# Kernel tuning notes

Hardware: AMD Instinct MI355X
Metric: run time of the kernel (lower is better)

## Reference

```python
import jax, jax.numpy as jnp
import numpy as np
from jax import lax

B, N, HID = 2, 2048, 2048
H, KVH, D = 16, 4, 128           # heads, kv heads, head_dim
GROUPS = H // KVH
FLA_WEIGHT = 0.01
NEG = -1e30


def setup_inputs() -> dict:
    key = jax.random.key(0)
    ks = jax.random.split(key, 5)
    s = 0.02
    return {
        "hidden_states": jax.random.normal(ks[0], (B, N, HID), jnp.float32),
        "Wq": jax.random.normal(ks[1], (HID, H * D), jnp.float32) * s,
        "Wk": jax.random.normal(ks[2], (HID, KVH * D), jnp.float32) * s,
        "Wv": jax.random.normal(ks[3], (HID, KVH * D), jnp.float32) * s,
        "Wo": jax.random.normal(ks[4], (H * D, HID), jnp.float32) * s,
    }


def _split_heads(x, h):
    b, n, _ = x.shape
    return x.reshape(b, n, h, -1).transpose(0, 2, 1, 3)  # b h n d


def _gla_attention(q, k, v, scale):
    # Gated linear attention: S_t = sigmoid(k_t) (.) S_{t-1} + k_t (x) v_t,
    # o_t = scale * q_t . S_t ; sequential recurrence over the seq dim.
    qs = jnp.moveaxis(q, 2, 0)  # n b h d
    ks = jnp.moveaxis(k, 2, 0)
    vs = jnp.moveaxis(v, 2, 0)

    def step(S, inp):
        qt, kt, vt = inp                                   # each (b,h,d)
        g = jax.nn.sigmoid(kt)                             # per-key-dim gate
        S = S * g[..., None] + kt[..., None] * vt[..., None, :]  # (b,h,d,dv)
        ot = scale * jnp.einsum('bhd,bhde->bhe', qt, S)
        return S, ot

    S0 = jnp.zeros(q.shape[:2] + (q.shape[-1], v.shape[-1]), q.dtype)
    _, o = lax.scan(step, S0, (qs, ks, vs))                # n b h dv
    return jnp.moveaxis(o, 0, 2)                           # b h n dv


def reference(hidden_states, Wq, Wk, Wv, Wo):
    scale = 1.0 / np.sqrt(D)
    q = _split_heads(hidden_states @ Wq, H)                # b h n d
    k = _split_heads(hidden_states @ Wk, KVH)
    v = _split_heads(hidden_states @ Wv, KVH)
    k = jnp.repeat(k, GROUPS, axis=1)                      # repeat_kv -> b H n d
    v = jnp.repeat(v, GROUPS, axis=1)

    # FLA branch
    fla = _gla_attention(q, k, v, scale)                   # b h n d
    fla = fla.transpose(0, 2, 1, 3).reshape(B, N, H * D)   # b n (h d)

    # Base causal softmax attention
    scores = jnp.einsum('bhnd,bhmd->bhnm', q, k) * scale
    causal = jnp.tril(jnp.ones((N, N), bool))
    scores = jnp.where(causal, scores, NEG)
    attn = jax.nn.softmax(scores, axis=-1)
    base = jnp.einsum('bhnm,bhmd->bhnd', attn, v)
    base = base.transpose(0, 2, 1, 3).reshape(B, N, H * D) @ Wo

    return base + FLA_WEIGHT * fla
```

## Files before the change

kernel.cpp:

```cpp
#include <hip/hip_runtime.h>
#include <hip/hip_bf16.h>
#include <cstdint>
#include <cstddef>


typedef __attribute__((ext_vector_type(4))) float f32x4;
typedef __attribute__((ext_vector_type(2))) float f32x2;
typedef __attribute__((ext_vector_type(8))) short s16x8;
typedef unsigned short u16;
typedef unsigned int u32;

__device__ __forceinline__ float bfu2f(u16 u) {
  union { unsigned int i; float f; } x; x.i = ((unsigned int)u) << 16; return x.f;
}
__device__ __forceinline__ u16 f2bfu(float f) {
  union { float f; unsigned int i; } x; x.f = f;
  unsigned int r = x.i + 0x7fffu + ((x.i >> 16) & 1u);
  return (u16)(r >> 16);
}
__device__ __forceinline__ void bf8_to_f(s16x8 v, float* o) {
  union { s16x8 v; u16 u[8]; } x; x.v = v;
#pragma unroll
  for (int j = 0; j < 8; j++) o[j] = bfu2f(x.u[j]);
}
__device__ __forceinline__ s16x8 pack_bf8(f32x4 lo, f32x4 hi) {
  union { s16x8 v; u16 u[8]; } x;
#pragma unroll
  for (int j = 0; j < 4; j++) { x.u[j] = f2bfu(lo[j]); x.u[4 + j] = f2bfu(hi[j]); }
  return x.v;
}
__device__ __forceinline__ void gload_lds16(const u16* g, u16* l) {
  __builtin_amdgcn_global_load_lds(
      (__attribute__((address_space(1))) void*)(g),
      (__attribute__((address_space(3))) void*)(l), 16, 0, 0);
}

__global__ __launch_bounds__(256) void f32_to_bf16(
    const float* __restrict__ src, u16* __restrict__ dst, int n8) {
  const int i = blockIdx.x * 256 + threadIdx.x;
  if (i < n8) {
    f32x4 a = *(const f32x4*)(src + (size_t)i * 8);
    f32x4 b = *(const f32x4*)(src + (size_t)i * 8 + 4);
    *(s16x8*)(dst + (size_t)i * 8) = pack_bf8(a, b);
  }
}

__global__ __launch_bounds__(256) void transpose_f32_bf16(
    const float* __restrict__ src, u16* __restrict__ dst, int R, int C) {
  __shared__ u16 tile[32][33];
  const int bx = blockIdx.x * 32, by = blockIdx.y * 32;
  const int tx = threadIdx.x & 31, ty = threadIdx.x >> 5;
#pragma unroll
  for (int i = 0; i < 32; i += 8)
    tile[ty + i][tx] = f2bfu(src[(size_t)(by + ty + i) * C + bx + tx]);
  __syncthreads();
#pragma unroll
  for (int i = 0; i < 32; i += 8)
    dst[(size_t)(bx + ty + i) * R + by + tx] = tile[tx][ty + i];
}

__global__ __launch_bounds__(256) void transpose_bf16(
    const u16* __restrict__ src, u16* __restrict__ dst, int R, int C) {
  __shared__ u16 tile[32][33];
  const int bx = blockIdx.x * 32, by = blockIdx.y * 32;
  const int tx = threadIdx.x & 31, ty = threadIdx.x >> 5;
#pragma unroll
  for (int i = 0; i < 32; i += 8)
    tile[ty + i][tx] = src[(size_t)(by + ty + i) * C + bx + tx];
  __syncthreads();
#pragma unroll
  for (int i = 0; i < 32; i += 8)
    dst[(size_t)(bx + ty + i) * R + by + tx] = tile[tx][ty + i];
}

__global__ __launch_bounds__(256) void gemm_qkv(
    const u16* __restrict__ A, const u16* __restrict__ WqT, const u16* __restrict__ WkT,
    const u16* __restrict__ WvT, u16* __restrict__ Qo, u16* __restrict__ Ko,
    u16* __restrict__ Vo) {
  __shared__ u16 Al[128 * 32];
  __shared__ u16 Bl[128 * 32];
  const int bx = blockIdx.x;
  const u16* Bt; u16* Cb; int n0, Nst;
  if (bx < 16)      { Bt = WqT; Cb = Qo; n0 = bx * 128;        Nst = 2048; }
  else if (bx < 20) { Bt = WkT; Cb = Ko; n0 = (bx - 16) * 128; Nst = 512; }
  else              { Bt = WvT; Cb = Vo; n0 = (bx - 20) * 128; Nst = 512; }
  const int K = 2048;
  const int m0 = blockIdx.y * 128;
  const int t = threadIdx.x, w = t >> 6, l = t & 63, lm = l & 15, lq = l >> 4;
  const int wr = w >> 1, wc = w & 1;
  const f32x4 z4 = {0.f, 0.f, 0.f, 0.f};
  f32x4 acc[4][4];
#pragma unroll
  for (int i = 0; i < 4; i++)
#pragma unroll
    for (int j = 0; j < 4; j++) acc[i][j] = z4;
  const int srow = l >> 2, scol = (l & 3) * 8;
  const u16* Ag = A + (size_t)(m0 + w * 32 + srow) * K + scol;
  const u16* Bg = Bt + (size_t)(n0 + w * 32 + srow) * K + scol;
  u16* Alw = &Al[(w * 32) * 32];
  u16* Blw = &Bl[(w * 32) * 32];
  for (int kk = 0; kk < K; kk += 32) {
    gload_lds16(Ag + kk, Alw);
    gload_lds16(Ag + (size_t)16 * K + kk, Alw + 16 * 32);
    gload_lds16(Bg + kk, Blw);
    gload_lds16(Bg + (size_t)16 * K + kk, Blw + 16 * 32);
    __syncthreads();
    s16x8 af[4], bfr[4];
#pragma unroll
    for (int sm = 0; sm < 4; sm++) af[sm] = *(const s16x8*)&Al[(wr * 64 + sm * 16 + lm) * 32 + lq * 8];
#pragma unroll
    for (int sn = 0; sn < 4; sn++) bfr[sn] = *(const s16x8*)&Bl[(wc * 64 + sn * 16 + lm) * 32 + lq * 8];
#pragma unroll
    for (int sm = 0; sm < 4; sm++)
#pragma unroll
      for (int sn = 0; sn < 4; sn++)
        acc[sm][sn] = __builtin_amdgcn_mfma_f32_16x16x32_bf16(af[sm], bfr[sn], acc[sm][sn], 0, 0, 0);
    __syncthreads();
  }
#pragma unroll
  for (int sm = 0; sm < 4; sm++)
#pragma unroll
    for (int sn = 0; sn < 4; sn++)
#pragma unroll
      for (int r = 0; r < 4; r++) {
        const int row = m0 + wr * 64 + sm * 16 + lq * 4 + r;
        const int col = n0 + wc * 64 + sn * 16 + lm;
        Cb[(size_t)row * Nst + col] = f2bfu(acc[sm][sn][r]);
      }
}

__global__ __launch_bounds__(512) void gemm_out2(
    const u16* __restrict__ A, const u16* __restrict__ Bt, float* __restrict__ Cf,
    const u16* __restrict__ addsrc) {
  __shared__ u16 Abuf[3 * 16384];
  __shared__ u16 Bbuf[3 * 8192];
  int f = blockIdx.y * 16 + blockIdx.x;
  f = (f & 7) * 32 + (f >> 3);
  const int by = f >> 4, bx = f & 15;
  const int m0 = by * 256, n0 = bx * 128;
  const int K = 2048, Nst = 2048;
  const int t = threadIdx.x, w = t >> 6, l = t & 63, lm = l & 15, lq = l >> 4;
  const int wr = w >> 1, wc = w & 1;
  const int tr = t >> 3, tc8 = (t & 7) * 8;
  const f32x4 z4 = {0.f, 0.f, 0.f, 0.f};
  f32x4 acc[4][4];
#pragma unroll
  for (int i = 0; i < 4; i++)
#pragma unroll
    for (int j = 0; j < 4; j++) acc[i][j] = z4;
  const u16* Ag = A + (size_t)m0 * K;
  const u16* Bg = Bt + (size_t)n0 * K;
  auto stage = [&](int kt, int bufi) {
#pragma unroll
    for (int i = 0; i < 4; i++) {
      const int row = i * 64 + tr;
      const int col = tc8 ^ ((row & 7) << 3);
      gload_lds16(Ag + (size_t)row * K + kt * 64 + col,
                  Abuf + bufi * 16384 + i * 4096 + w * 512);
    }
#pragma unroll
    for (int i = 0; i < 2; i++) {
      const int row = i * 64 + tr;
      const int col = tc8 ^ ((row & 7) << 3);
      gload_lds16(Bg + (size_t)row * K + kt * 64 + col,
                  Bbuf + bufi * 8192 + i * 4096 + w * 512);
    }
  };
  const int nt = K >> 6;
  stage(0, 0);
  stage(1, 1);
  int cur = 0;
#pragma unroll 1
  for (int kt = 0; kt < nt; kt++) {
    if (kt + 2 < nt) {
      int nb = cur + 2; if (nb >= 3) nb -= 3;
      stage(kt + 2, nb);
      asm volatile("s_waitcnt vmcnt(12)" ::: "memory");
    } else if (kt + 1 < nt) {
      asm volatile("s_waitcnt vmcnt(6)" ::: "memory");
    } else {
      asm volatile("s_waitcnt vmcnt(0)" ::: "memory");
    }
    __builtin_amdgcn_s_barrier();
    const u16* Ab = Abuf + cur * 16384;
    const u16* Bb = Bbuf + cur * 8192;
    s16x8 af[4][2], bff[4][2];
#pragma unroll
    for (int sm = 0; sm < 4; sm++) {
      const int row = wr * 64 + sm * 16 + lm;
#pragma unroll
      for (int kk = 0; kk < 2; kk++)
        af[sm][kk] = *(const s16x8*)&Ab[row * 64 +
            ((((kk << 6) | (lq << 4)) ^ ((row & 7) << 4)) >> 1)];
    }
#pragma unroll
    for (int sn = 0; sn < 4; sn++) {
      const int row = wc * 64 + sn * 16 + lm;
#pragma unroll
      for (int kk = 0; kk < 2; kk++)
        bff[sn][kk] = *(const s16x8*)&Bb[row * 64 +
            ((((kk << 6) | (lq << 4)) ^ ((row & 7) << 4)) >> 1)];
    }
#pragma unroll
    for (int kk = 0; kk < 2; kk++)
#pragma unroll
      for (int sm = 0; sm < 4; sm++)
#pragma unroll
        for (int sn = 0; sn < 4; sn++)
          acc[sm][sn] = __builtin_amdgcn_mfma_f32_16x16x32_bf16(
              af[sm][kk], bff[sn][kk], acc[sm][sn], 0, 0, 0);
    asm volatile("s_waitcnt lgkmcnt(0)" ::: "memory");
    __builtin_amdgcn_s_barrier();
    cur = (cur == 2) ? 0 : cur + 1;
  }
#pragma unroll
  for (int sm = 0; sm < 4; sm++)
#pragma unroll
    for (int sn = 0; sn < 4; sn++)
#pragma unroll
      for (int r = 0; r < 4; r++) {
        const int row = m0 + wr * 64 + sm * 16 + lq * 4 + r;
        const int col = n0 + wc * 64 + sn * 16 + lm;
        float v = acc[sm][sn][r] + 0.01f * bfu2f(addsrc[(size_t)row * Nst + col]);
        Cf[(size_t)row * Nst + col] = v;
      }
}

__global__ __launch_bounds__(512) void flash_attn_wave(
    const u16* __restrict__ Q, const u16* __restrict__ Kx,
    const u16* __restrict__ Vt, u16* __restrict__ AO) {
  __shared__ u16 Klds[2][64 * 128];
  __shared__ u16 Vlds[2][128 * 64];
  __shared__ u16 Pl[8][16][68];
  const int bid = blockIdx.x;
  const int set = bid & 7;
  const int b = set >> 2, kvh = set & 3;
  const int rest = bid >> 3;
  const int j0 = rest >> 1, hp = rest & 1;
  const int t = threadIdx.x, w = t >> 6, l = t & 63, lm = l & 15, lq = l >> 4;
  const int h = kvh * 4 + hp * 2 + (w & 1);
  const int cs = (w >> 1) & 1, mh = w >> 2;
  const float scale = 0.0883883476483184f;
  const u16* Kbase = Kx + (size_t)(b * 2048) * 512 + kvh * 128;
  const u16* Vbase = Vt + (size_t)(b * 512 + kvh * 128) * 2048;
  const f32x4 z4 = {0.f, 0.f, 0.f, 0.f};

  auto stage = [&](int kt, int bufi) {
    const int key0 = kt * 64;
#pragma unroll
    for (int r = 0; r < 2; r++) {
      const int row = r * 32 + w * 4 + (l >> 4);
      const int scb = ((l & 15) * 16) ^ ((row & 7) << 4);
      gload_lds16(Kbase + (size_t)(key0 + row) * 512 + (scb >> 1),
                  &Klds[bufi][r * 4096 + w * 512]);
    }
#pragma unroll
    for (int r = 0; r < 2; r++) {
      const int row = r * 64 + w * 8 + (l >> 3);
      const int scb = ((l & 7) * 16) ^ ((row & 7) << 4);
      gload_lds16(Vbase + (size_t)row * 2048 + key0 + (scb >> 1),
                  &Vlds[bufi][r * 4096 + w * 512]);
    }
  };

#pragma unroll 1
  for (int ph = 0; ph < 2; ph++) {
    const int j = ph ? (31 - j0) : j0;
    const int c = 2 * j + cs;
    const int base = c * 32;
    int cur = 0;
    stage(0, 0);
    s16x8 qf[4];
#pragma unroll
    for (int kk = 0; kk < 4; kk++)
      qf[kk] = *(const s16x8*)(Q + ((size_t)(b * 2048 + base + mh * 16 + lm)) * 2048 +
                               h * 128 + kk * 32 + lq * 8);
    f32x4 oacc[8];
#pragma unroll
    for (int e = 0; e < 8; e++) oacc[e] = z4;
    float lsum[4] = {0.f, 0.f, 0.f, 0.f};
#pragma unroll 1
    for (int kt = 0; kt <= j; kt++) {
      const int key0 = kt * 64;
      if (kt < j) {
        stage(kt + 1, cur ^ 1);
        asm volatile("s_waitcnt vmcnt(4)" ::: "memory");
      } else {
        asm volatile("s_waitcnt vmcnt(0)" ::: "memory");
      }
      __builtin_amdgcn_s_barrier();
      const char* KB = (const char*)&Klds[cur][0];
      const char* VB = (const char*)&Vlds[cur][0];
      s16x8 kf[4][4];
#pragma unroll
      for (int nst = 0; nst < 4; nst++)
#pragma unroll
        for (int kk = 0; kk < 4; kk++) {
          const int row = nst * 16 + lm;
          const int cb = (kk * 64 + lq * 16) ^ ((row & 7) << 4);
          kf[nst][kk] = *(const s16x8*)(KB + row * 256 + cb);
        }
      f32x4 sacc[4];
#pragma unroll
      for (int i = 0; i < 4; i++) sacc[i] = z4;
#pragma unroll
      for (int nst = 0; nst < 4; nst++)
#pragma unroll
        for (int kk = 0; kk < 4; kk++)
          sacc[nst] = __builtin_amdgcn_mfma_f32_16x16x32_bf16(
              qf[kk], kf[nst][kk], sacc[nst], 0, 0, 0);
      const bool diag = (kt == j);
#pragma unroll
      for (int r = 0; r < 4; r++) {
        const int qrow = base + mh * 16 + lq * 4 + r;
#pragma unroll
        for (int nst = 0; nst < 4; nst++) {
          float pv = __expf(sacc[nst][r] * scale);
          if (diag && (key0 + nst * 16 + lm > qrow)) pv = 0.f;
          lsum[r] += pv;
          Pl[w][lq * 4 + r][nst * 16 + lm] = f2bfu(pv);
        }
      }
      s16x8 vf[8][2];
#pragma unroll
      for (int et = 0; et < 8; et++)
#pragma unroll
        for (int kc = 0; kc < 2; kc++) {
          const int row = et * 16 + lm;
          const int cb = (kc * 64 + lq * 16) ^ ((row & 7) << 4);
          vf[et][kc] = *(const s16x8*)(VB + row * 128 + cb);
        }
      s16x8 pf[2];
#pragma unroll
      for (int kc = 0; kc < 2; kc++)
        pf[kc] = *(const s16x8*)&Pl[w][lm][kc * 32 + lq * 8];
#pragma unroll
      for (int et = 0; et < 8; et++)
#pragma unroll
        for (int kc = 0; kc < 2; kc++)
          oacc[et] = __builtin_amdgcn_mfma_f32_16x16x32_bf16(
              pf[kc], vf[et][kc], oacc[et], 0, 0, 0);
      asm volatile("s_waitcnt lgkmcnt(0)" ::: "memory");
      __builtin_amdgcn_s_barrier();
      cur ^= 1;
    }
#pragma unroll
    for (int r = 0; r < 4; r++) {
#pragma unroll
      for (int off = 1; off < 16; off <<= 1)
        lsum[r] += __shfl_xor(lsum[r], off, 64);
    }
#pragma unroll
    for (int r = 0; r < 4; r++) {
      const float inv = 1.f / lsum[r];
      const int row = base + mh * 16 + lq * 4 + r;
      u16* op = AO + ((size_t)(b * 2048 + row)) * 2048 + h * 128;
#pragma unroll
      for (int et = 0; et < 8; et++) op[et * 16 + lm] = f2bfu(oacc[et][r] * inv);
    }
  }
}

__global__ __launch_bounds__(256) void fla_contrib32(
    const u16* __restrict__ Kx, const u16* __restrict__ Vt,
    u16* __restrict__ Gg, u16* __restrict__ Ktg, u16* __restrict__ MT,
    float* __restrict__ Lam) {
  __shared__ float gl[32][132];
  __shared__ float kl[32][132];
  __shared__ float ktl[32][132];
  __shared__ u16 khT[128][40];
  const int c = blockIdx.x, kvh = blockIdx.y, b = blockIdx.z;
  const int bk = b * 4 + kvh;
  const int t = threadIdx.x;
  const size_t cb = (size_t)bk * 64 + c;
  {
    const int r = t >> 3, c0 = (t & 7) * 16;
    const u16* kp = Kx + ((size_t)(b * 2048 + c * 32 + r)) * 512 + kvh * 128 + c0;
#pragma unroll
    for (int i = 0; i < 2; i++) {
      float kv[8];
      bf8_to_f(*(const s16x8*)(kp + i * 8), kv);
#pragma unroll
      for (int j = 0; j < 8; j++) {
        kl[r][c0 + i * 8 + j] = kv[j];
        gl[r][c0 + i * 8 + j] = 1.f / (1.f + __expf(-kv[j]));
      }
    }
  }
  __syncthreads();
  if (t < 128) {
    float G = 1.f;
#pragma unroll
    for (int s = 0; s < 32; s++) {
      G *= gl[s][t];
      gl[s][t] = G;
      ktl[s][t] = kl[s][t] / G;
    }
    Lam[cb * 128 + t] = G;
    const float lam = G;
#pragma unroll
    for (int s = 0; s < 32; s++) khT[t][s] = f2bfu(ktl[s][t] * lam);
  }
  __syncthreads();
  {
    const int r = t >> 3, c0 = (t & 7) * 16;
    u16* gp = Gg + cb * 4096 + r * 128 + c0;
    u16* kp = Ktg + cb * 4096 + r * 128 + c0;
#pragma unroll
    for (int i = 0; i < 2; i++) {
      f32x4 a = *(f32x4*)&gl[r][c0 + i * 8];
      f32x4 b2 = *(f32x4*)&gl[r][c0 + i * 8 + 4];
      *(s16x8*)(gp + i * 8) = pack_bf8(a, b2);
      a = *(f32x4*)&ktl[r][c0 + i * 8];
      b2 = *(f32x4*)&ktl[r][c0 + i * 8 + 4];
      *(s16x8*)(kp + i * 8) = pack_bf8(a, b2);
    }
  }
  const int w = t >> 6, l = t & 63, lm = l & 15, lq = l >> 4;
  const f32x4 z4 = {0.f, 0.f, 0.f, 0.f};
  f32x4 macc[2][8];
#pragma unroll
  for (int ei = 0; ei < 2; ei++)
#pragma unroll
    for (int dt = 0; dt < 8; dt++) macc[ei][dt] = z4;
  s16x8 vtf[2];
#pragma unroll
  for (int ei = 0; ei < 2; ei++) {
    const int et = w * 2 + ei;
    vtf[ei] = *(const s16x8*)(Vt + ((size_t)(b * 512 + kvh * 128 + et * 16 + lm)) * 2048 +
                              c * 32 + lq * 8);
  }
#pragma unroll
  for (int dt = 0; dt < 8; dt++) {
    s16x8 kf = *(const s16x8*)&khT[dt * 16 + lm][lq * 8];
#pragma unroll
    for (int ei = 0; ei < 2; ei++)
      macc[ei][dt] = __builtin_amdgcn_mfma_f32_16x16x32_bf16(vtf[ei], kf, macc[ei][dt], 0, 0, 0);
  }
  u16* mp = MT + cb * 16384;
#pragma unroll
  for (int ei = 0; ei < 2; ei++)
#pragma unroll
    for (int dt = 0; dt < 8; dt++)
#pragma unroll
      for (int r = 0; r < 4; r++)
        mp[(size_t)((w * 2 + ei) * 16 + lq * 4 + r) * 128 + dt * 16 + lm] =
            f2bfu(macc[ei][dt][r]);
}

__global__ __launch_bounds__(256) void fla_prefix32(
    const u16* __restrict__ MT, const float* __restrict__ Lam, u16* __restrict__ SwsT) {
  const int eg = blockIdx.x, bk = blockIdx.y;
  const int t = threadIdx.x;
  const int e = eg * 4 + (t >> 6), d0 = (t & 63) * 2;
  const size_t cb0 = (size_t)bk * 64;
  const u16* mp = MT + cb0 * 16384 + e * 128 + d0;
  const float* lp = Lam + cb0 * 128 + d0;
  u16* sp = SwsT + cb0 * 16384 + e * 128 + d0;
  float s0 = 0.f, s1 = 0.f;
  u32 mnext = *(const u32*)mp;
  f32x2 lnext = *(const f32x2*)lp;
#pragma unroll 1
  for (int c = 0; c < 64; c++) {
    const u32 mcur = mnext;
    const f32x2 lcur = lnext;
    if (c < 63) {
      mnext = *(const u32*)(mp + (size_t)(c + 1) * 16384);
      lnext = *(const f32x2*)(lp + (size_t)(c + 1) * 128);
    }
    *(u32*)(sp + (size_t)c * 16384) = (u32)f2bfu(s0) | ((u32)f2bfu(s1) << 16);
    s0 = s0 * lcur[0] + bfu2f((u16)(mcur & 0xffffu));
    s1 = s1 * lcur[1] + bfu2f((u16)(mcur >> 16));
  }
}

__global__ __launch_bounds__(256) void fla_output_mfma(
    const u16* __restrict__ Q, const u16* __restrict__ Gg, const u16* __restrict__ Ktg,
    const u16* __restrict__ SwsT, const u16* __restrict__ Vt, u16* __restrict__ Fla) {
  __shared__ u16 Pl[4][2][16][40];
  const int c = blockIdx.x, h = blockIdx.y, b = blockIdx.z;
  const int kvh = h >> 2, bk = b * 4 + kvh;
  const int t = threadIdx.x, w = t >> 6, l = t & 63, lm = l & 15, lq = l >> 4;
  const float scale = 0.0883883476483184f;
  const size_t cb = (size_t)bk * 64 + c;
  const f32x4 z4 = {0.f, 0.f, 0.f, 0.f};
  s16x8 qgf[2][4];
#pragma unroll
  for (int m = 0; m < 2; m++)
#pragma unroll
    for (int kk = 0; kk < 4; kk++) {
      float qv[8], gv[8];
      bf8_to_f(*(const s16x8*)(Q + ((size_t)(b * 2048 + c * 32 + m * 16 + lm)) * 2048 +
                               h * 128 + kk * 32 + lq * 8), qv);
      bf8_to_f(*(const s16x8*)(Gg + cb * 4096 + (m * 16 + lm) * 128 + kk * 32 + lq * 8), gv);
      f32x4 a, b2;
#pragma unroll
      for (int j = 0; j < 4; j++) { a[j] = qv[j] * gv[j]; b2[j] = qv[4 + j] * gv[4 + j]; }
      qgf[m][kk] = pack_bf8(a, b2);
    }
  f32x4 sacc[2][2];
#pragma unroll
  for (int m = 0; m < 2; m++)
#pragma unroll
    for (int st = 0; st < 2; st++) sacc[m][st] = z4;
#pragma unroll
  for (int st = 0; st < 2; st++)
#pragma unroll
    for (int kk = 0; kk < 4; kk++) {
      s16x8 ktf = *(const s16x8*)(Ktg + cb * 4096 + (st * 16 + lm) * 128 + kk * 32 + lq * 8);
#pragma unroll
      for (int m = 0; m < 2; m++)
        sacc[m][st] = __builtin_amdgcn_mfma_f32_16x16x32_bf16(qgf[m][kk], ktf, sacc[m][st], 0, 0, 0);
    }
#pragma unroll
  for (int m = 0; m < 2; m++)
#pragma unroll
    for (int st = 0; st < 2; st++)
#pragma unroll
      for (int r = 0; r < 4; r++) {
        const int trow = m * 16 + lq * 4 + r;
        const int scol = st * 16 + lm;
        Pl[w][m][lq * 4 + r][st * 16 + lm] = f2bfu(scol <= trow ? sacc[m][st][r] : 0.f);
      }
  s16x8 pf[2];
#pragma unroll
  for (int m = 0; m < 2; m++) pf[m] = *(const s16x8*)&Pl[w][m][lm][lq * 8];
  f32x4 oacc[2][2];
#pragma unroll
  for (int m = 0; m < 2; m++)
#pragma unroll
    for (int ei = 0; ei < 2; ei++) oacc[m][ei] = z4;
#pragma unroll
  for (int ei = 0; ei < 2; ei++) {
    const int et = w * 2 + ei;
    s16x8 vtf = *(const s16x8*)(Vt + ((size_t)(b * 512 + kvh * 128 + et * 16 + lm)) * 2048 +
                                c * 32 + lq * 8);
#pragma unroll
    for (int m = 0; m < 2; m++)
      oacc[m][ei] = __builtin_amdgcn_mfma_f32_16x16x32_bf16(pf[m], vtf, oacc[m][ei], 0, 0, 0);
#pragma unroll
    for (int kk = 0; kk < 4; kk++) {
      s16x8 s0f = *(const s16x8*)(SwsT + cb * 16384 + (et * 16 + lm) * 128 + kk * 32 + lq * 8);
#pragma unroll
      for (int m = 0; m < 2; m++)
        oacc[m][ei] = __builtin_amdgcn_mfma_f32_16x16x32_bf16(qgf[m][kk], s0f, oacc[m][ei], 0, 0, 0);
    }
  }
#pragma unroll
  for (int m = 0; m < 2; m++)
#pragma unroll
    for (int ei = 0; ei < 2; ei++)
#pragma unroll
      for (int r = 0; r < 4; r++)
        Fla[((size_t)(b * 2048 + c * 32 + m * 16 + lq * 4 + r)) * 2048 + h * 128 +
            (w * 2 + ei) * 16 + lm] = f2bfu(scale * oacc[m][ei][r]);
}

extern "C" void kernel_launch(void* const* d_in, const int* in_sizes, int n_in,
                              void* d_out, int out_size, void* d_ws, size_t ws_size,
                              hipStream_t stream) {
  const float* X  = (const float*)d_in[0];
  const float* Wq = (const float*)d_in[1];
  const float* Wk = (const float*)d_in[2];
  const float* Wv = (const float*)d_in[3];
  const float* Wo = (const float*)d_in[4];
  float* out = (float*)d_out;

  char* ws = (char*)d_ws;
  size_t off = 0;
  auto alloc = [&](size_t bytes) { void* p = ws + off; off += (bytes + 255) & ~(size_t)255; return p; };
  u16* WoT = (u16*)alloc(2048ull * 2048 * 2);
  u16* Qb  = (u16*)alloc(4096ull * 2048 * 2);
  u16* Kb  = (u16*)alloc(4096ull * 512 * 2);
  u16* Vb  = (u16*)alloc(4096ull * 512 * 2);
  u16* Vtb = (u16*)alloc(2ull * 512 * 2048 * 2);
  u16* Fla = (u16*)alloc(4096ull * 2048 * 2);
  u16* SH16 = (u16*)alloc(4096ull * 2048 * 2);
  u16* Xb = SH16;
  u16* MT = SH16;
  u16* AO = SH16;
  char* BIG = (char*)alloc(26ull * 1024 * 1024);
  u16* WqT = (u16*)BIG;
  u16* WkT = (u16*)(BIG + 8ull * 1024 * 1024);
  u16* WvT = (u16*)(BIG + 10ull * 1024 * 1024);
  u16* Gg   = (u16*)BIG;
  u16* Ktg  = (u16*)(BIG + 4194304ull);
  u16* SwsT = (u16*)(BIG + 8388608ull);
  float* Lam = (float*)(BIG + 8388608ull + 16777216ull);
  (void)ws_size; (void)in_sizes; (void)n_in; (void)out_size;

  dim3 blk(256);
  f32_to_bf16<<<dim3(4096), blk, 0, stream>>>(X, Xb, 4096 * 2048 / 8);
  transpose_f32_bf16<<<dim3(64, 64), blk, 0, stream>>>(Wq, WqT, 2048, 2048);
  transpose_f32_bf16<<<dim3(16, 64), blk, 0, stream>>>(Wk, WkT, 2048, 512);
  transpose_f32_bf16<<<dim3(16, 64), blk, 0, stream>>>(Wv, WvT, 2048, 512);
  transpose_f32_bf16<<<dim3(64, 64), blk, 0, stream>>>(Wo, WoT, 2048, 2048);

  gemm_qkv<<<dim3(24, 32), blk, 0, stream>>>(Xb, WqT, WkT, WvT, Qb, Kb, Vb);

  transpose_bf16<<<dim3(16, 64), blk, 0, stream>>>(Vb, Vtb, 2048, 512);
  transpose_bf16<<<dim3(16, 64), blk, 0, stream>>>(Vb + 2048ull * 512, Vtb + 512ull * 2048, 2048, 512);

  fla_contrib32<<<dim3(64, 4, 2), blk, 0, stream>>>(Kb, Vtb, Gg, Ktg, MT, Lam);
  fla_prefix32<<<dim3(32, 8), blk, 0, stream>>>(MT, Lam, SwsT);
  fla_output_mfma<<<dim3(64, 16, 2), blk, 0, stream>>>(Qb, Gg, Ktg, SwsT, Vtb, Fla);

  flash_attn_wave<<<dim3(256), dim3(512), 0, stream>>>(Qb, Kb, Vtb, AO);

  gemm_out2<<<dim3(16, 16), dim3(512), 0, stream>>>(AO, WoT, out, Fla);
}
```

Before: 363.6 us.

## Split flash attention into 256-thread blocks per head and unroll prefix scan

Each flash attention block now handles one query head with 4 waves instead of two heads with 8 waves, and the grid doubles to 512 blocks. The aim is more blocks per CU, better latency hiding and better balance, at the cost of loading each K/V tile twice as often. The softmax exponent switches from __expf to exp2f with the scale folded into a log2(e) multiplier. The prefix-scan kernel is unrolled by two with two chunks prefetched ahead, to overlap its loads with the serial recurrence.

```diff
diff --git a/kernel.cpp b/kernel.cpp
--- a/kernel.cpp
+++ b/kernel.cpp
@@ -226,21 +226,22 @@
       }
 }
 
-__global__ __launch_bounds__(512) void flash_attn_wave(
+__global__ __launch_bounds__(256) void flash_attn_wave(
     const u16* __restrict__ Q, const u16* __restrict__ Kx,
     const u16* __restrict__ Vt, u16* __restrict__ AO) {
   __shared__ u16 Klds[2][64 * 128];
   __shared__ u16 Vlds[2][128 * 64];
-  __shared__ u16 Pl[8][16][68];
+  __shared__ u16 Pl[4][16][68];
   const int bid = blockIdx.x;
   const int set = bid & 7;
   const int b = set >> 2, kvh = set & 3;
   const int rest = bid >> 3;
-  const int j0 = rest >> 1, hp = rest & 1;
+  const int j0 = rest & 15;
+  const int hpq = rest >> 4;
   const int t = threadIdx.x, w = t >> 6, l = t & 63, lm = l & 15, lq = l >> 4;
-  const int h = kvh * 4 + hp * 2 + (w & 1);
-  const int cs = (w >> 1) & 1, mh = w >> 2;
-  const float scale = 0.0883883476483184f;
+  const int h = kvh * 4 + hpq;
+  const int cs = w & 1, mh = w >> 1;
+  const float scale2 = 0.127517827f;
   const u16* Kbase = Kx + (size_t)(b * 2048) * 512 + kvh * 128;
   const u16* Vbase = Vt + (size_t)(b * 512 + kvh * 128) * 2048;
   const f32x4 z4 = {0.f, 0.f, 0.f, 0.f};
@@ -248,18 +249,18 @@
   auto stage = [&](int kt, int bufi) {
     const int key0 = kt * 64;
 #pragma unroll
-    for (int r = 0; r < 2; r++) {
-      const int row = r * 32 + w * 4 + (l >> 4);
+    for (int r = 0; r < 4; r++) {
+      const int row = r * 16 + w * 4 + (l >> 4);
       const int scb = ((l & 15) * 16) ^ ((row & 7) << 4);
       gload_lds16(Kbase + (size_t)(key0 + row) * 512 + (scb >> 1),
-                  &Klds[bufi][r * 4096 + w * 512]);
-    }
-#pragma unroll
-    for (int r = 0; r < 2; r++) {
-      const int row = r * 64 + w * 8 + (l >> 3);
+                  &Klds[bufi][r * 2048 + w * 512]);
+    }
+#pragma unroll
+    for (int r = 0; r < 4; r++) {
+      const int row = r * 32 + w * 8 + (l >> 3);
       const int scb = ((l & 7) * 16) ^ ((row & 7) << 4);
       gload_lds16(Vbase + (size_t)row * 2048 + key0 + (scb >> 1),
-                  &Vlds[bufi][r * 4096 + w * 512]);
+                  &Vlds[bufi][r * 2048 + w * 512]);
     }
   };
 
@@ -284,7 +285,7 @@
       const int key0 = kt * 64;
       if (kt < j) {
         stage(kt + 1, cur ^ 1);
-        asm volatile("s_waitcnt vmcnt(4)" ::: "memory");
+        asm volatile("s_waitcnt vmcnt(8)" ::: "memory");
       } else {
         asm volatile("s_waitcnt vmcnt(0)" ::: "memory");
       }
@@ -315,7 +316,7 @@
         const int qrow = base + mh * 16 + lq * 4 + r;
 #pragma unroll
         for (int nst = 0; nst < 4; nst++) {
-          float pv = __expf(sacc[nst][r] * scale);
+          float pv = exp2f(sacc[nst][r] * scale2);
           if (diag && (key0 + nst * 16 + lm > qrow)) pv = 0.f;
           lsum[r] += pv;
           Pl[w][lq * 4 + r][nst * 16 + lm] = f2bfu(pv);
@@ -458,19 +459,27 @@
   const float* lp = Lam + cb0 * 128 + d0;
   u16* sp = SwsT + cb0 * 16384 + e * 128 + d0;
   float s0 = 0.f, s1 = 0.f;
-  u32 mnext = *(const u32*)mp;
-  f32x2 lnext = *(const f32x2*)lp;
+  u32 ma = *(const u32*)mp;
+  u32 mb = *(const u32*)(mp + 16384);
+  f32x2 la = *(const f32x2*)lp;
+  f32x2 lb = *(const f32x2*)(lp + 128);
 #pragma unroll 1
-  for (int c = 0; c < 64; c++) {
-    const u32 mcur = mnext;
-    const f32x2 lcur = lnext;
-    if (c < 63) {
-      mnext = *(const u32*)(mp + (size_t)(c + 1) * 16384);
-      lnext = *(const f32x2*)(lp + (size_t)(c + 1) * 128);
+  for (int c = 0; c < 64; c += 2) {
+    u32 na = 0, nb = 0;
+    f32x2 nla = {0.f, 0.f}, nlb = {0.f, 0.f};
+    if (c + 2 < 64) {
+      na = *(const u32*)(mp + (size_t)(c + 2) * 16384);
+      nla = *(const f32x2*)(lp + (size_t)(c + 2) * 128);
+      nb = *(const u32*)(mp + (size_t)(c + 3) * 16384);
+      nlb = *(const f32x2*)(lp + (size_t)(c + 3) * 128);
     }
     *(u32*)(sp + (size_t)c * 16384) = (u32)f2bfu(s0) | ((u32)f2bfu(s1) << 16);
-    s0 = s0 * lcur[0] + bfu2f((u16)(mcur & 0xffffu));
-    s1 = s1 * lcur[1] + bfu2f((u16)(mcur >> 16));
+    s0 = s0 * la[0] + bfu2f((u16)(ma & 0xffffu));
+    s1 = s1 * la[1] + bfu2f((u16)(ma >> 16));
+    *(u32*)(sp + (size_t)(c + 1) * 16384) = (u32)f2bfu(s0) | ((u32)f2bfu(s1) << 16);
+    s0 = s0 * lb[0] + bfu2f((u16)(mb & 0xffffu));
+    s1 = s1 * lb[1] + bfu2f((u16)(mb >> 16));
+    ma = na; mb = nb; la = nla; lb = nlb;
   }
 }
 
@@ -605,7 +614,7 @@
   fla_prefix32<<<dim3(32, 8), blk, 0, stream>>>(MT, Lam, SwsT);
   fla_output_mfma<<<dim3(64, 16, 2), blk, 0, stream>>>(Qb, Gg, Ktg, SwsT, Vtb, Fla);
 
-  flash_attn_wave<<<dim3(256), dim3(512), 0, stream>>>(Qb, Kb, Vtb, AO);
+  flash_attn_wave<<<dim3(512), dim3(256), 0, stream>>>(Qb, Kb, Vtb, AO);
 
   gemm_out2<<<dim3(16, 16), dim3(512), 0, stream>>>(AO, WoT, out, Fla);
 }
```

Measured after the change: 360.7 us. No clear change (-0.8%).
